# Optimization experiments

Hardware: AMD Instinct MI355X
Metric: run time of the kernel (lower is better)

The kernel has to match this reference:

```python
import jax, jax.numpy as jnp
import numpy as np

B, C_IN, H_IMG, W_IMG = 64, 384, 32, 32
D, HEADS = 768, 12
HD = D // HEADS
GS = 16            # attention grid = image_size // 2
ET = 1             # extra tokens
N = GS * GS + ET   # 257
MLP_H = 4 * D
EPS = 1e-5


def _rel_index():
    coords = np.stack(np.meshgrid(np.arange(GS), np.arange(GS), indexing='ij'))  # [2,GS,GS]
    cf = coords.reshape(2, -1)                      # [2, GS*GS]
    rel = (cf[:, :, None] - cf[:, None, :]).transpose(1, 2, 0)  # [P,P,2]
    rel[:, :, 0] += GS - 1
    rel[:, :, 1] += GS - 1
    rel[:, :, 0] *= 2 * GS - 1
    idx = rel.sum(-1)                               # [P,P]
    out = np.zeros((N, N), dtype=np.int32)          # F.pad with zeros for extra tokens
    out[ET:, ET:] = idx
    return out

REL_IDX = jnp.asarray(_rel_index())


def _ln(x, g, b):
    m = x.mean(-1, keepdims=True)
    v = ((x - m) ** 2).mean(-1, keepdims=True)
    return (x - m) / jnp.sqrt(v + EPS) * g + b


def setup_inputs() -> dict:
    key = jax.random.key(0)
    ks = jax.random.split(key, 16)
    s = 0.02
    return {
        "x": jax.random.normal(ks[0], (B, C_IN, H_IMG, W_IMG), jnp.float32),
        "H": 32,
        "W": 32,
        "geo_bias": jax.random.normal(ks[1], (1, N, D), jnp.float32),
        "extra_token": jax.random.normal(ks[2], (1, ET, D), jnp.float32) * s,
        "conv_w": jax.random.normal(ks[3], (D, C_IN, 3, 3), jnp.float32) * np.sqrt(2.0 / (9 * D)),
        "conv_b": jnp.zeros((D,), jnp.float32),
        "pe_g": jnp.ones((D,), jnp.float32),
        "pe_b": jnp.zeros((D,), jnp.float32),
        "n1_g": jnp.ones((D,), jnp.float32),
        "n1_b": jnp.zeros((D,), jnp.float32),
        "qkv_w": jax.random.normal(ks[4], (3 * D, D), jnp.float32) * s,
        "rpb_table": jax.random.normal(ks[5], ((2 * GS - 1) * (2 * GS - 1), HEADS), jnp.float32) * s,
        "proj_w": jax.random.normal(ks[6], (D, D), jnp.float32) * s,
        "proj_b": jnp.zeros((D,), jnp.float32),
        "n2_g": jnp.ones((D,), jnp.float32),
        "n2_b": jnp.zeros((D,), jnp.float32),
        "fc1_w": jax.random.normal(ks[7], (MLP_H, D), jnp.float32) * s,
        "fc1_b": jnp.zeros((MLP_H,), jnp.float32),
        "fc2_w": jax.random.normal(ks[8], (D, MLP_H), jnp.float32) * s,
        "fc2_b": jnp.zeros((D,), jnp.float32),
    }


def reference(x, H, W, geo_bias, extra_token, conv_w, conv_b, pe_g, pe_b,
              n1_g, n1_b, qkv_w, rpb_table, proj_w, proj_b, n2_g, n2_b,
              fc1_w, fc1_b, fc2_w, fc2_b):
    # OverlapPatchEmbed: conv k3 s2 p1 -> [B, D, GS, GS]
    y = jax.lax.conv_general_dilated(x, conv_w, (2, 2), ((1, 1), (1, 1)),
                                     dimension_numbers=('NCHW', 'OIHW', 'NCHW'))
    y = y + conv_b[None, :, None, None]
    y = y.reshape(B, D, GS * GS).transpose(0, 2, 1)   # [B, P, D]
    y = _ln(y, pe_g, pe_b)
    tok = jnp.broadcast_to(extra_token, (B, ET, D))
    y = jnp.concatenate([tok, y], axis=1) + geo_bias  # [B, N, D]

    # Relative attention
    h = _ln(y, n1_g, n1_b)
    qkv = (h @ qkv_w.T).reshape(B, N, 3, HEADS, HD).transpose(2, 0, 3, 1, 4)
    q, k, v = qkv[0] * (HD ** -0.5), qkv[1], qkv[2]   # [B, h, N, d]
    attn = jnp.einsum('bhnd,bhmd->bhnm', q, k)
    bias = rpb_table[REL_IDX].transpose(2, 0, 1)      # [heads, N, N]
    attn = jax.nn.softmax(attn + bias[None], axis=-1)
    o = jnp.einsum('bhnm,bhmd->bhnd', attn, v).transpose(0, 2, 1, 3).reshape(B, N, D)
    y = y + (o @ proj_w.T + proj_b)

    # MLP
    h2 = _ln(y, n2_g, n2_b)
    h2 = jax.nn.gelu(h2 @ fc1_w.T + fc1_b, approximate=False)
    y = y + (h2 @ fc2_w.T + fc2_b)
    return y
```

## Files before the change

### kernel.cpp

```cpp
#include <hip/hip_runtime.h>
#include <hip/hip_bf16.h>
#include <cstdint>

using bf16 = __hip_bfloat16;
typedef __attribute__((ext_vector_type(8))) short short8;
typedef __attribute__((ext_vector_type(4))) float f32x4;


__device__ __forceinline__ void gld_lds16(const bf16* g, bf16* l) {
  __builtin_amdgcn_global_load_lds(
      (const __attribute__((address_space(1))) void*)g,
      (__attribute__((address_space(3))) void*)l, 16, 0, 0);
}

__device__ __forceinline__ unsigned short f2bf_bits(float f) {
  uint32_t u = __builtin_bit_cast(uint32_t, f);
  uint32_t r = (u + 0x7fffu + ((u >> 16) & 1u)) >> 16;
  return (unsigned short)r;
}

__device__ __forceinline__ int xcd_swz(int bid, int nwg) {
  const int q = nwg >> 3, r = nwg & 7;
  const int x = bid & 7, o = bid >> 3;
  return (x < r ? x * (q + 1) : r * (q + 1) + (x - r) * q) + o;
}

__global__ void castf2b(const float* __restrict__ in, bf16* __restrict__ out, int n) {
  int i = blockIdx.x * blockDim.x + threadIdx.x;
  int st = gridDim.x * blockDim.x;
  for (; i < n; i += st) out[i] = __float2bfloat16(in[i]);
}

__global__ void zero_b(bf16* __restrict__ p, int n) {
  int i = blockIdx.x * blockDim.x + threadIdx.x;
  if (i < n) p[i] = __float2bfloat16(0.f);
}

__global__ void convw_reorder(const float* __restrict__ w, bf16* __restrict__ o) {
  int i = blockIdx.x * blockDim.x + threadIdx.x;
  if (i >= 768 * 3456) return;
  int n = i / 3456, r = i % 3456;
  int tap = r / 384, c = r % 384;
  o[i] = __float2bfloat16(w[(long)n * 3456 + c * 9 + tap]);
}

__global__ __launch_bounds__(256, 4)
void nhwc_kernel(const float* __restrict__ x, bf16* __restrict__ xp) {
  __shared__ bf16 T[384 * 33];
  const int biy = blockIdx.x;
  const int b = biy >> 5, iy = biy & 31;
  const int tid = threadIdx.x;
  const int ix = tid & 31, cp = tid >> 5;
  const long xrow = (long)b * 384 * 1024 + iy * 32 + ix;
#pragma unroll
  for (int t = 0; t < 48; ++t) {
    const int c = t * 8 + cp;
    T[c * 33 + ix] = __float2bfloat16(x[xrow + (long)c * 1024]);
  }
  __syncthreads();
  bf16* dst = xp + (((long)b * 34 + iy + 1) * 34 + 1) * 384;
  for (int e4 = tid; e4 < 3072; e4 += 256) {
    const int e = e4 * 4;
    const int ixr = e / 384, c = e % 384;
    ushort4 v;
    v.x = ((const unsigned short*)T)[(c + 0) * 33 + ixr];
    v.y = ((const unsigned short*)T)[(c + 1) * 33 + ixr];
    v.z = ((const unsigned short*)T)[(c + 2) * 33 + ixr];
    v.w = ((const unsigned short*)T)[(c + 3) * 33 + ixr];
    *(ushort4*)(dst + e) = v;
  }
}

template <int EPI>
__global__ __launch_bounds__(256, 2)
void gemm_bt(const bf16* __restrict__ A, const bf16* __restrict__ Bw,
             const float* __restrict__ bias, float* __restrict__ outf,
             bf16* __restrict__ outb, int N, int K, int Mreal, int ntn)
{
  __shared__ bf16 As[128 * 64];
  __shared__ bf16 Bs[128 * 64];
  const int bid = xcd_swz(blockIdx.x, gridDim.x);
  const int mt = bid / ntn, nt = bid % ntn;
  const int tid = threadIdx.x;
  const int lane = tid & 63, wave = tid >> 6;
  const int wm = wave >> 1, wn = wave & 1;
  const int lr = lane & 15, lk = (lane >> 4) * 8;

  f32x4 acc[4][4];
#pragma unroll
  for (int i = 0; i < 4; ++i)
#pragma unroll
    for (int j = 0; j < 4; ++j) acc[i][j] = (f32x4){0.f, 0.f, 0.f, 0.f};

  const int arow = tid >> 3;
  const int acol = (tid & 7) * 8;
  const bf16* ag = A + ((long)mt * 128 + arow) * K + acol;
  const bf16* bg = Bw + ((long)nt * 128 + arow) * K + acol;

  for (int k0 = 0; k0 < K; k0 += 64) {
#pragma unroll
    for (int j = 0; j < 4; ++j)
      gld_lds16(ag + (long)(j * 32) * K + k0, &As[(j * 256 + tid) * 8]);
#pragma unroll
    for (int j = 0; j < 4; ++j)
      gld_lds16(bg + (long)(j * 32) * K + k0, &Bs[(j * 256 + tid) * 8]);
    __syncthreads();
#pragma unroll
    for (int ks = 0; ks < 2; ++ks) {
      short8 af[4], bv[4];
#pragma unroll
      for (int i = 0; i < 4; ++i)
        af[i] = *(const short8*)&As[(wm * 64 + i * 16 + lr) * 64 + ks * 32 + lk];
#pragma unroll
      for (int i = 0; i < 4; ++i)
        bv[i] = *(const short8*)&Bs[(wn * 64 + i * 16 + lr) * 64 + ks * 32 + lk];
#pragma unroll
      for (int i = 0; i < 4; ++i)
#pragma unroll
        for (int j = 0; j < 4; ++j)
          acc[i][j] = __builtin_amdgcn_mfma_f32_16x16x32_bf16(af[i], bv[j], acc[i][j], 0, 0, 0);
    }
    __syncthreads();
  }

  const int rbase = mt * 128 + wm * 64 + (lane >> 4) * 4;
  const int cbase = nt * 128 + wn * 64 + lr;
#pragma unroll
  for (int i = 0; i < 4; ++i) {
#pragma unroll
    for (int j = 0; j < 4; ++j) {
      const int col = cbase + j * 16;
      float bvv = 0.f;
      if constexpr (EPI != 0) bvv = bias[col];
#pragma unroll
      for (int r = 0; r < 4; ++r) {
        const int row = rbase + i * 16 + r;
        const float v = acc[i][j][r];
        if constexpr (EPI == 0) {
          outb[(long)row * N + col] = __float2bfloat16(v);
        } else if constexpr (EPI == 1) {
          outb[(long)row * N + col] = __float2bfloat16(v + bvv);
        } else if constexpr (EPI == 2) {
          const float t = v + bvv;
          outb[(long)row * N + col] =
              __float2bfloat16(0.5f * t * (1.0f + erff(t * 0.70710678118f)));
        } else {
          if (row < Mreal) {
            const long o = (long)row * N + col;
            outf[o] = outf[o] + v + bvv;
          }
        }
      }
    }
  }
}

__global__ __launch_bounds__(256, 2)
void conv_gemm(const bf16* __restrict__ xp, const bf16* __restrict__ Bw,
               const float* __restrict__ bias, bf16* __restrict__ outb)
{
  __shared__ bf16 As[128 * 64];
  __shared__ bf16 Bs[128 * 64];
  const int bid = xcd_swz(blockIdx.x, gridDim.x);
  const int mt = bid / 6, nt = bid % 6;
  const int tid = threadIdx.x;
  const int lane = tid & 63, wave = tid >> 6;
  const int wm = wave >> 1, wn = wave & 1;
  const int lr = lane & 15, lk = (lane >> 4) * 8;

  f32x4 acc[4][4];
#pragma unroll
  for (int i = 0; i < 4; ++i)
#pragma unroll
    for (int j = 0; j < 4; ++j) acc[i][j] = (f32x4){0.f, 0.f, 0.f, 0.f};

  const int arow = tid >> 3;
  const int acol = (tid & 7) * 8;
  long abase[4];
#pragma unroll
  for (int j = 0; j < 4; ++j) {
    const int m = mt * 128 + j * 32 + arow;
    const int b = m >> 8, p = m & 255;
    const int gy = p >> 4, gx = p & 15;
    abase[j] = (((long)b * 34 + 2 * gy) * 34 + 2 * gx) * 384 + acol;
  }
  const bf16* bg = Bw + ((long)nt * 128 + arow) * 3456 + acol;

#pragma unroll 1
  for (int tap = 0; tap < 9; ++tap) {
    const int toff = ((tap / 3) * 34 + (tap % 3)) * 384;
#pragma unroll 1
    for (int kc = 0; kc < 384; kc += 64) {
      const int k0 = tap * 384 + kc;
#pragma unroll
      for (int j = 0; j < 4; ++j)
        gld_lds16(xp + abase[j] + toff + kc, &As[(j * 256 + tid) * 8]);
#pragma unroll
      for (int j = 0; j < 4; ++j)
        gld_lds16(bg + (long)(j * 32) * 3456 + k0, &Bs[(j * 256 + tid) * 8]);
      __syncthreads();
#pragma unroll
      for (int ks = 0; ks < 2; ++ks) {
        short8 af[4], bv[4];
#pragma unroll
        for (int i = 0; i < 4; ++i)
          af[i] = *(const short8*)&As[(wm * 64 + i * 16 + lr) * 64 + ks * 32 + lk];
#pragma unroll
        for (int i = 0; i < 4; ++i)
          bv[i] = *(const short8*)&Bs[(wn * 64 + i * 16 + lr) * 64 + ks * 32 + lk];
#pragma unroll
        for (int i = 0; i < 4; ++i)
#pragma unroll
          for (int j = 0; j < 4; ++j)
            acc[i][j] = __builtin_amdgcn_mfma_f32_16x16x32_bf16(af[i], bv[j], acc[i][j], 0, 0, 0);
      }
      __syncthreads();
    }
  }

  const int rbase = mt * 128 + wm * 64 + (lane >> 4) * 4;
  const int cbase = nt * 128 + wn * 64 + lr;
#pragma unroll
  for (int i = 0; i < 4; ++i) {
#pragma unroll
    for (int j = 0; j < 4; ++j) {
      const int col = cbase + j * 16;
      const float bvv = bias[col];
#pragma unroll
      for (int r = 0; r < 4; ++r) {
        const int row = rbase + i * 16 + r;
        outb[(long)row * 768 + col] = __float2bfloat16(acc[i][j][r] + bvv);
      }
    }
  }
}

__global__ __launch_bounds__(256, 4)
void embed_kernel(const bf16* __restrict__ CO, const float* __restrict__ extra,
                  const float* __restrict__ geo, const float* __restrict__ pe_g,
                  const float* __restrict__ pe_b, float* __restrict__ y)
{
  const int row = blockIdx.x;
  const int b = row / 257, t = row % 257;
  const int tid = threadIdx.x;
  if (t == 0) {
#pragma unroll
    for (int u = 0; u < 3; ++u) {
      const int d = tid + u * 256;
      y[(long)row * 768 + d] = extra[d] + geo[d];
    }
    return;
  }
  const bf16* src = CO + (long)(b * 256 + (t - 1)) * 768;
  float v[3]; float s = 0.f, s2 = 0.f;
#pragma unroll
  for (int u = 0; u < 3; ++u) {
    v[u] = __bfloat162float(src[tid + u * 256]);
    s += v[u]; s2 += v[u] * v[u];
  }
#pragma unroll
  for (int off = 32; off > 0; off >>= 1) { s += __shfl_xor(s, off); s2 += __shfl_xor(s2, off); }
  __shared__ float red[2][4];
  const int wave = tid >> 6, lane = tid & 63;
  if (lane == 0) { red[0][wave] = s; red[1][wave] = s2; }
  __syncthreads();
  const float S = red[0][0] + red[0][1] + red[0][2] + red[0][3];
  const float S2 = red[1][0] + red[1][1] + red[1][2] + red[1][3];
  const float mean = S * (1.f / 768.f);
  const float var = S2 * (1.f / 768.f) - mean * mean;
  const float rinv = rsqrtf(var + 1e-5f);
#pragma unroll
  for (int u = 0; u < 3; ++u) {
    const int d = tid + u * 256;
    y[(long)row * 768 + d] = (v[u] - mean) * rinv * pe_g[d] + pe_b[d] + geo[(long)t * 768 + d];
  }
}

__global__ __launch_bounds__(256, 4)
void ln_kernel(const float* __restrict__ y, const float* __restrict__ g,
               const float* __restrict__ bta, bf16* __restrict__ H, int Mreal)
{
  const int row = blockIdx.x;
  const int tid = threadIdx.x;
  if (row >= Mreal) {
#pragma unroll
    for (int u = 0; u < 3; ++u) H[(long)row * 768 + tid + u * 256] = __float2bfloat16(0.f);
    return;
  }
  const float* src = y + (long)row * 768;
  float v[3]; float s = 0.f, s2 = 0.f;
#pragma unroll
  for (int u = 0; u < 3; ++u) { v[u] = src[tid + u * 256]; s += v[u]; s2 += v[u] * v[u]; }
#pragma unroll
  for (int off = 32; off > 0; off >>= 1) { s += __shfl_xor(s, off); s2 += __shfl_xor(s2, off); }
  __shared__ float red[2][4];
  const int wave = tid >> 6, lane = tid & 63;
  if (lane == 0) { red[0][wave] = s; red[1][wave] = s2; }
  __syncthreads();
  const float S = red[0][0] + red[0][1] + red[0][2] + red[0][3];
  const float S2 = red[1][0] + red[1][1] + red[1][2] + red[1][3];
  const float mean = S * (1.f / 768.f);
  const float var = S2 * (1.f / 768.f) - mean * mean;
  const float rinv = rsqrtf(var + 1e-5f);
#pragma unroll
  for (int u = 0; u < 3; ++u) {
    const int d = tid + u * 256;
    H[(long)row * 768 + d] = __float2bfloat16((v[u] - mean) * rinv * g[d] + bta[d]);
  }
}

__global__ void rpbT_kernel(const float* __restrict__ rpb, float* __restrict__ rpbT) {
  int i = blockIdx.x * blockDim.x + threadIdx.x;
  if (i >= 12 * 961) return;
  int h = i / 961, t = i % 961;
  rpbT[i] = rpb[t * 12 + h];
}

__global__ __launch_bounds__(256, 2)
void vtrans_kernel(const bf16* __restrict__ qkv, bf16* __restrict__ vt) {
  __shared__ bf16 Vl[257 * 65];
  const int bh = blockIdx.x;
  const int b = bh / 12, h = bh % 12;
  const long src = (long)b * 257 * 2304 + 1536 + h * 64;
  for (int e = threadIdx.x; e < 257 * 64; e += 256) {
    const int t = e >> 6, d = e & 63;
    Vl[t * 65 + d] = qkv[src + (long)t * 2304 + d];
  }
  __syncthreads();
  const bf16 z = __float2bfloat16(0.f);
  const long dst = (long)bh * 64 * 320;
  for (int e = threadIdx.x; e < 64 * 320; e += 256) {
    const int d = e / 320, tp = e % 320;
    vt[dst + e] = (tp < 257) ? Vl[tp * 65 + d] : z;
  }
}

__global__ __launch_bounds__(256, 2)
void attn_mfma(const bf16* __restrict__ qkv, const bf16* __restrict__ vt,
               const float* __restrict__ rpbT, bf16* __restrict__ O)
{
  __shared__ bf16 Ks[64 * 64];
  __shared__ bf16 Vts[64 * 64];
  __shared__ float rpb_s[961];
  __shared__ bf16 Pl[4][16 * 72];

  const int bid = blockIdx.x;
  const int qb = bid % 5;
  const int bh = bid / 5;
  const int h = bh % 12, b = bh / 12;
  const int tid = threadIdx.x;
  const int lane = tid & 63, w = tid >> 6;
  const int lr = lane & 15, g = lane >> 4;

  for (int t = tid; t < 961; t += 256) rpb_s[t] = rpbT[h * 961 + t];

  const long qkv_bh = (long)b * 257 * 2304 + h * 64;
  const long vt_bh = (long)bh * 64 * 320;

  const int q_tok = qb * 64 + w * 16 + lr;
  const bf16* qp = qkv + qkv_bh + (long)q_tok * 2304;
  short8 qf[2];
  qf[0] = *(const short8*)(qp + g * 8);
  qf[1] = *(const short8*)(qp + 32 + g * 8);

  f32x4 ao[4];
#pragma unroll
  for (int df = 0; df < 4; ++df) ao[df] = (f32x4){0.f, 0.f, 0.f, 0.f};
  float mval = -1e30f, l = 0.f;

  for (int ck = 0; ck < 5; ++ck) {
    const int c0 = ck * 64;
#pragma unroll
    for (int it = 0; it < 2; ++it) {
      const int beta = it * 256 + tid;
      const int row = beta >> 3, cb = beta & 7;
      const int cbs = cb ^ (row & 7);
      gld_lds16(qkv + qkv_bh + (long)(c0 + row) * 2304 + 768 + cbs * 8, &Ks[beta * 8]);
      gld_lds16(vt + vt_bh + (long)row * 320 + c0 + cbs * 8, &Vts[beta * 8]);
    }
    __syncthreads();

    f32x4 st[4];
#pragma unroll
    for (int kf = 0; kf < 4; ++kf) st[kf] = (f32x4){0.f, 0.f, 0.f, 0.f};
#pragma unroll
    for (int ks = 0; ks < 2; ++ks) {
#pragma unroll
      for (int kf = 0; kf < 4; ++kf) {
        const int row = kf * 16 + lr;
        const short8 kfrag = *(const short8*)&Ks[row * 64 + ((ks * 4 + g) ^ (row & 7)) * 8];
        st[kf] = __builtin_amdgcn_mfma_f32_16x16x32_bf16(kfrag, qf[ks], st[kf], 0, 0, 0);
      }
    }

    float p[4][4];
    float t = -1e30f;
#pragma unroll
    for (int kf = 0; kf < 4; ++kf) {
#pragma unroll
      for (int r = 0; r < 4; ++r) {
        const int key = c0 + kf * 16 + g * 4 + r;
        float s;
        if (key < 257) {
          int idx = 0;
          if (q_tok > 0 && key > 0) {
            const int qi = q_tok - 1, kj = key - 1;
            idx = ((qi >> 4) - (kj >> 4) + 15) * 31 + ((qi & 15) - (kj & 15) + 15);
            idx = idx < 0 ? 0 : (idx > 960 ? 960 : idx);
          }
          s = 0.125f * st[kf][r] + rpb_s[idx];
        } else {
          s = -1e30f;
        }
        p[kf][r] = s;
        t = fmaxf(t, s);
      }
    }
    t = fmaxf(t, __shfl_xor(t, 16));
    t = fmaxf(t, __shfl_xor(t, 32));
    const float mnew = fmaxf(mval, t);
    const float corr = __expf(mval - mnew);
    mval = mnew;
    float ps = 0.f;
#pragma unroll
    for (int kf = 0; kf < 4; ++kf)
#pragma unroll
      for (int r = 0; r < 4; ++r) { p[kf][r] = __expf(p[kf][r] - mnew); ps += p[kf][r]; }
    ps += __shfl_xor(ps, 16);
    ps += __shfl_xor(ps, 32);
    l = l * corr + ps;

#pragma unroll
    for (int r = 0; r < 4; ++r) {
      const float cr = __shfl(corr, g * 4 + r);
#pragma unroll
      for (int df = 0; df < 4; ++df) ao[df][r] *= cr;
    }

    bf16* plw = &Pl[w][0];
#pragma unroll
    for (int kf = 0; kf < 4; ++kf) {
      uint2 pw;
      pw.x = ((uint32_t)f2bf_bits(p[kf][1]) << 16) | (uint32_t)f2bf_bits(p[kf][0]);
      pw.y = ((uint32_t)f2bf_bits(p[kf][3]) << 16) | (uint32_t)f2bf_bits(p[kf][2]);
      *(uint2*)&plw[lr * 72 + kf * 16 + g * 4] = pw;
    }

#pragma unroll
    for (int ks = 0; ks < 2; ++ks) {
      const short8 pa = *(const short8*)&plw[lr * 72 + ks * 32 + g * 8];
#pragma unroll
      for (int df = 0; df < 4; ++df) {
        const int row = df * 16 + lr;
        const short8 vfrag = *(const short8*)&Vts[row * 64 + ((ks * 4 + g) ^ (row & 7)) * 8];
        ao[df] = __builtin_amdgcn_mfma_f32_16x16x32_bf16(pa, vfrag, ao[df], 0, 0, 0);
      }
    }
    __syncthreads();
  }

  const float rl = 1.0f / l;
#pragma unroll
  for (int r = 0; r < 4; ++r) {
    const float rr = __shfl(rl, g * 4 + r);
    const int qg = qb * 64 + w * 16 + g * 4 + r;
    if (qg < 257) {
      bf16* op = O + ((long)b * 257 + qg) * 768 + h * 64;
#pragma unroll
      for (int df = 0; df < 4; ++df)
        op[df * 16 + lr] = __float2bfloat16(ao[df][r] * rr);
    }
  }
}


extern "C" void kernel_launch(void* const* d_in, const int* in_sizes, int n_in,
                              void* d_out, int out_size, void* d_ws, size_t ws_size,
                              hipStream_t stream) {
  (void)in_sizes; (void)n_in; (void)out_size;
  const float* x      = (const float*)d_in[0];
  const float* geo    = (const float*)d_in[3];
  const float* extra  = (const float*)d_in[4];
  const float* conv_w = (const float*)d_in[5];
  const float* conv_b = (const float*)d_in[6];
  const float* pe_g   = (const float*)d_in[7];
  const float* pe_b   = (const float*)d_in[8];
  const float* n1_g   = (const float*)d_in[9];
  const float* n1_b   = (const float*)d_in[10];
  const float* qkv_w  = (const float*)d_in[11];
  const float* rpb    = (const float*)d_in[12];
  const float* proj_w = (const float*)d_in[13];
  const float* proj_b = (const float*)d_in[14];
  const float* n2_g   = (const float*)d_in[15];
  const float* n2_b   = (const float*)d_in[16];
  const float* fc1_w  = (const float*)d_in[17];
  const float* fc1_b  = (const float*)d_in[18];
  const float* fc2_w  = (const float*)d_in[19];
  const float* fc2_b  = (const float*)d_in[20];
  float* out = (float*)d_out;

  constexpr size_t SZ_WCONV = 768UL * 3456 * 2;
  constexpr size_t SZ_WQKV  = 2304UL * 768 * 2;
  constexpr size_t SZ_WPROJ = 768UL * 768 * 2;
  constexpr size_t SZ_WFC1  = 3072UL * 768 * 2;
  constexpr size_t SZ_WFC2  = 768UL * 3072 * 2;
  constexpr size_t SZ_H     = 16512UL * 768 * 2;
  constexpr size_t SZ_A     = 16384UL * 3456 * 2;
  constexpr size_t SZ_B     = 16512UL * 768 * 2;
  constexpr size_t TOTAL = SZ_WCONV + SZ_WQKV + SZ_WPROJ + SZ_WFC1 + SZ_WFC2 + SZ_H + SZ_A + SZ_B;
  if (ws_size < TOTAL) return;

  char* ws = (char*)d_ws;
  bf16* Wconv = (bf16*)ws;                    ws += SZ_WCONV;
  bf16* Wqkv  = (bf16*)ws;                    ws += SZ_WQKV;
  bf16* Wproj = (bf16*)ws;                    ws += SZ_WPROJ;
  bf16* Wfc1  = (bf16*)ws;                    ws += SZ_WFC1;
  bf16* Wfc2  = (bf16*)ws;                    ws += SZ_WFC2;
  bf16* Hb    = (bf16*)ws;                    ws += SZ_H;
  char* regA  = ws;                           ws += SZ_A;
  char* regB  = ws;
  bf16* XP   = (bf16*)regA;
  bf16* QKV  = (bf16*)regA;
  bf16* MLPH = (bf16*)regA;
  constexpr size_t SZ_QKV = 16512UL * 2304 * 2;
  constexpr size_t SZ_XP  = 64UL * 34 * 34 * 384 * 2;
  bf16* Vt   = (bf16*)(regA + SZ_QKV);
  bf16* CO   = (bf16*)regB;
  bf16* Oat  = (bf16*)regB;
  float* rpbTp = (float*)Hb;

  convw_reorder<<<10368, 256, 0, stream>>>(conv_w, Wconv);
  castf2b<<<2048, 256, 0, stream>>>(qkv_w,  Wqkv, 1769472);
  castf2b<<<1024, 256, 0, stream>>>(proj_w, Wproj, 589824);
  castf2b<<<2048, 256, 0, stream>>>(fc1_w,  Wfc1, 2359296);
  castf2b<<<2048, 256, 0, stream>>>(fc2_w,  Wfc2, 2359296);
  hipMemsetAsync(XP, 0, SZ_XP, stream);
  nhwc_kernel<<<2048, 256, 0, stream>>>(x, XP);
  conv_gemm<<<128 * 6, 256, 0, stream>>>(XP, Wconv, conv_b, CO);
  embed_kernel<<<16448, 256, 0, stream>>>(CO, extra, geo, pe_g, pe_b, out);
  ln_kernel<<<16512, 256, 0, stream>>>(out, n1_g, n1_b, Hb, 16448);
  gemm_bt<0><<<129 * 18, 256, 0, stream>>>(Hb, Wqkv, nullptr, nullptr, QKV, 2304, 768, 16448, 18);
  rpbT_kernel<<<46, 256, 0, stream>>>(rpb, rpbTp);
  vtrans_kernel<<<768, 256, 0, stream>>>(QKV, Vt);
  zero_b<<<192, 256, 0, stream>>>(Oat + 16448L * 768, 49152);
  attn_mfma<<<3840, 256, 0, stream>>>(QKV, Vt, rpbTp, Oat);
  gemm_bt<3><<<129 * 6, 256, 0, stream>>>(Oat, Wproj, proj_b, out, nullptr, 768, 768, 16448, 6);
  ln_kernel<<<16512, 256, 0, stream>>>(out, n2_g, n2_b, Hb, 16448);
  gemm_bt<2><<<129 * 24, 256, 0, stream>>>(Hb, Wfc1, fc1_b, nullptr, MLPH, 3072, 768, 16448, 24);
  gemm_bt<3><<<129 * 6, 256, 0, stream>>>(MLPH, Wfc2, fc2_b, out, nullptr, 768, 3072, 16448, 6);
}
```

Before: 735.4 us.

## Double-buffer LDS tiles and XOR-swizzle layout in GEMM and conv kernels

New measurement: 749.4 us. Within noise of the previous version (+1.9%).

```diff
diff --git a/kernel.cpp b/kernel.cpp
--- a/kernel.cpp
+++ b/kernel.cpp
@@ -77,14 +77,14 @@
              const float* __restrict__ bias, float* __restrict__ outf,
              bf16* __restrict__ outb, int N, int K, int Mreal, int ntn)
 {
-  __shared__ bf16 As[128 * 64];
-  __shared__ bf16 Bs[128 * 64];
+  __shared__ bf16 As[2][128 * 64];
+  __shared__ bf16 Bs[2][128 * 64];
   const int bid = xcd_swz(blockIdx.x, gridDim.x);
   const int mt = bid / ntn, nt = bid % ntn;
   const int tid = threadIdx.x;
   const int lane = tid & 63, wave = tid >> 6;
   const int wm = wave >> 1, wn = wave & 1;
-  const int lr = lane & 15, lk = (lane >> 4) * 8;
+  const int lr = lane & 15, lg = lane >> 4;
 
   f32x4 acc[4][4];
 #pragma unroll
@@ -93,33 +93,50 @@
     for (int j = 0; j < 4; ++j) acc[i][j] = (f32x4){0.f, 0.f, 0.f, 0.f};
 
   const int arow = tid >> 3;
-  const int acol = (tid & 7) * 8;
-  const bf16* ag = A + ((long)mt * 128 + arow) * K + acol;
-  const bf16* bg = Bw + ((long)nt * 128 + arow) * K + acol;
-
-  for (int k0 = 0; k0 < K; k0 += 64) {
-#pragma unroll
-    for (int j = 0; j < 4; ++j)
-      gld_lds16(ag + (long)(j * 32) * K + k0, &As[(j * 256 + tid) * 8]);
-#pragma unroll
-    for (int j = 0; j < 4; ++j)
-      gld_lds16(bg + (long)(j * 32) * K + k0, &Bs[(j * 256 + tid) * 8]);
-    __syncthreads();
+  const int scol = (((tid & 7) ^ (arow & 7))) * 8;
+  const bf16* ag = A + ((long)mt * 128 + arow) * K + scol;
+  const bf16* bg = Bw + ((long)nt * 128 + arow) * K + scol;
+
+  auto stage = [&](int kt, int buf) {
+    const int k0 = kt << 6;
+#pragma unroll
+    for (int j = 0; j < 4; ++j) {
+      gld_lds16(ag + (long)(j * 32) * K + k0, &As[buf][(j * 256 + tid) * 8]);
+      gld_lds16(bg + (long)(j * 32) * K + k0, &Bs[buf][(j * 256 + tid) * 8]);
+    }
+  };
+  auto compute = [&](int buf) {
 #pragma unroll
     for (int ks = 0; ks < 2; ++ks) {
       short8 af[4], bv[4];
 #pragma unroll
-      for (int i = 0; i < 4; ++i)
-        af[i] = *(const short8*)&As[(wm * 64 + i * 16 + lr) * 64 + ks * 32 + lk];
-#pragma unroll
-      for (int i = 0; i < 4; ++i)
-        bv[i] = *(const short8*)&Bs[(wn * 64 + i * 16 + lr) * 64 + ks * 32 + lk];
+      for (int i = 0; i < 4; ++i) {
+        const int ra = wm * 64 + i * 16 + lr;
+        af[i] = *(const short8*)&As[buf][ra * 64 + (((ks * 4 + lg) ^ (ra & 7)) * 8)];
+      }
+#pragma unroll
+      for (int i = 0; i < 4; ++i) {
+        const int rb = wn * 64 + i * 16 + lr;
+        bv[i] = *(const short8*)&Bs[buf][rb * 64 + (((ks * 4 + lg) ^ (rb & 7)) * 8)];
+      }
 #pragma unroll
       for (int i = 0; i < 4; ++i)
 #pragma unroll
         for (int j = 0; j < 4; ++j)
           acc[i][j] = __builtin_amdgcn_mfma_f32_16x16x32_bf16(af[i], bv[j], acc[i][j], 0, 0, 0);
     }
+  };
+
+  const int nk = K >> 6;
+  stage(0, 0);
+  __syncthreads();
+  for (int t = 0; t < nk; t += 2) {
+    if (t + 1 < nk) stage(t + 1, 1);
+    compute(0);
+    __syncthreads();
+    if (t + 1 >= nk) break;
+    if (t + 2 < nk) stage(t + 2, 0);
+    compute(1);
     __syncthreads();
   }
 
@@ -159,14 +176,14 @@
 void conv_gemm(const bf16* __restrict__ xp, const bf16* __restrict__ Bw,
                const float* __restrict__ bias, bf16* __restrict__ outb)
 {
-  __shared__ bf16 As[128 * 64];
-  __shared__ bf16 Bs[128 * 64];
+  __shared__ bf16 As[2][128 * 64];
+  __shared__ bf16 Bs[2][128 * 64];
   const int bid = xcd_swz(blockIdx.x, gridDim.x);
   const int mt = bid / 6, nt = bid % 6;
   const int tid = threadIdx.x;
   const int lane = tid & 63, wave = tid >> 6;
   const int wm = wave >> 1, wn = wave & 1;
-  const int lr = lane & 15, lk = (lane >> 4) * 8;
+  const int lr = lane & 15, lg = lane >> 4;
 
   f32x4 acc[4][4];
 #pragma unroll
@@ -175,47 +192,57 @@
     for (int j = 0; j < 4; ++j) acc[i][j] = (f32x4){0.f, 0.f, 0.f, 0.f};
 
   const int arow = tid >> 3;
-  const int acol = (tid & 7) * 8;
+  const int scol = (((tid & 7) ^ (arow & 7))) * 8;
   long abase[4];
 #pragma unroll
   for (int j = 0; j < 4; ++j) {
     const int m = mt * 128 + j * 32 + arow;
     const int b = m >> 8, p = m & 255;
     const int gy = p >> 4, gx = p & 15;
-    abase[j] = (((long)b * 34 + 2 * gy) * 34 + 2 * gx) * 384 + acol;
-  }
-  const bf16* bg = Bw + ((long)nt * 128 + arow) * 3456 + acol;
-
-#pragma unroll 1
-  for (int tap = 0; tap < 9; ++tap) {
-    const int toff = ((tap / 3) * 34 + (tap % 3)) * 384;
-#pragma unroll 1
-    for (int kc = 0; kc < 384; kc += 64) {
-      const int k0 = tap * 384 + kc;
-#pragma unroll
-      for (int j = 0; j < 4; ++j)
-        gld_lds16(xp + abase[j] + toff + kc, &As[(j * 256 + tid) * 8]);
-#pragma unroll
-      for (int j = 0; j < 4; ++j)
-        gld_lds16(bg + (long)(j * 32) * 3456 + k0, &Bs[(j * 256 + tid) * 8]);
-      __syncthreads();
-#pragma unroll
-      for (int ks = 0; ks < 2; ++ks) {
-        short8 af[4], bv[4];
-#pragma unroll
-        for (int i = 0; i < 4; ++i)
-          af[i] = *(const short8*)&As[(wm * 64 + i * 16 + lr) * 64 + ks * 32 + lk];
-#pragma unroll
-        for (int i = 0; i < 4; ++i)
-          bv[i] = *(const short8*)&Bs[(wn * 64 + i * 16 + lr) * 64 + ks * 32 + lk];
-#pragma unroll
-        for (int i = 0; i < 4; ++i)
-#pragma unroll
-          for (int j = 0; j < 4; ++j)
-            acc[i][j] = __builtin_amdgcn_mfma_f32_16x16x32_bf16(af[i], bv[j], acc[i][j], 0, 0, 0);
-      }
-      __syncthreads();
-    }
+    abase[j] = (((long)b * 34 + 2 * gy) * 34 + 2 * gx) * 384 + scol;
+  }
+  const bf16* bg = Bw + ((long)nt * 128 + arow) * 3456 + scol;
+
+  auto stage = [&](int kidx, int buf) {
+    const int tap = kidx / 6, kc = (kidx % 6) * 64;
+    const int toff = ((tap / 3) * 34 + (tap % 3)) * 384 + kc;
+#pragma unroll
+    for (int j = 0; j < 4; ++j) {
+      gld_lds16(xp + abase[j] + toff, &As[buf][(j * 256 + tid) * 8]);
+      gld_lds16(bg + (long)(j * 32) * 3456 + kidx * 64, &Bs[buf][(j * 256 + tid) * 8]);
+    }
+  };
+  auto compute = [&](int buf) {
+#pragma unroll
+    for (int ks = 0; ks < 2; ++ks) {
+      short8 af[4], bv[4];
+#pragma unroll
+      for (int i = 0; i < 4; ++i) {
+        const int ra = wm * 64 + i * 16 + lr;
+        af[i] = *(const short8*)&As[buf][ra * 64 + (((ks * 4 + lg) ^ (ra & 7)) * 8)];
+      }
+#pragma unroll
+      for (int i = 0; i < 4; ++i) {
+        const int rb = wn * 64 + i * 16 + lr;
+        bv[i] = *(const short8*)&Bs[buf][rb * 64 + (((ks * 4 + lg) ^ (rb & 7)) * 8)];
+      }
+#pragma unroll
+      for (int i = 0; i < 4; ++i)
+#pragma unroll
+        for (int j = 0; j < 4; ++j)
+          acc[i][j] = __builtin_amdgcn_mfma_f32_16x16x32_bf16(af[i], bv[j], acc[i][j], 0, 0, 0);
+    }
+  };
+
+  stage(0, 0);
+  __syncthreads();
+  for (int t = 0; t < 54; t += 2) {
+    if (t + 1 < 54) stage(t + 1, 1);
+    compute(0);
+    __syncthreads();
+    if (t + 2 < 54) stage(t + 2, 0);
+    compute(1);
+    __syncthreads();
   }
 
   const int rbase = mt * 128 + wm * 64 + (lane >> 4) * 4;
```
